# Optimization experiments

Measured on AMD Instinct MI355X. Metric: run time of the kernel, lower is better.

Reference implementation:

```python
import jax, jax.numpy as jnp
import numpy as np

B, H, W, D, DFF = 32, 40, 40, 128, 2048
S = H * W  # 1600
BN_EPS = 1e-5


def setup_inputs() -> dict:
    key = jax.random.key(0)
    ks = jax.random.split(key, 8)
    se = jax.random.normal(ks[2], (H, W, H, W), dtype=jnp.float32)
    se = se + jnp.transpose(se, (2, 3, 0, 1))  # symmetric init as in torch code
    wscale = 0.02
    return {
        "tgt": jax.random.normal(ks[0], (B, H, W, D), dtype=jnp.float32),
        "memory": jax.random.normal(ks[1], (B, H, W, D), dtype=jnp.float32),
        "score_embed": se,
        "w1": jax.random.normal(ks[3], (D, D), dtype=jnp.float32) * wscale,
        "b1": jnp.zeros((D,), jnp.float32),
        "g1": jnp.ones((2 * S,), jnp.float32),
        "be1": jnp.zeros((2 * S,), jnp.float32),
        "w2": jax.random.normal(ks[4], (DFF, 2 * S), dtype=jnp.float32) * wscale,
        "b2": jnp.zeros((DFF,), jnp.float32),
        "g2": jnp.ones((DFF,), jnp.float32),
        "be2": jnp.zeros((DFF,), jnp.float32),
        "w3": jax.random.normal(ks[5], (1, DFF), dtype=jnp.float32) * wscale,
        "b3": jnp.zeros((1,), jnp.float32),
        "g3": jnp.ones((1,), jnp.float32),
        "be3": jnp.zeros((1,), jnp.float32),
    }


def _bn_eval(x, gamma, beta):
    # BatchNorm eval mode with running_mean=0, running_var=1 (as initialized)
    return x * (gamma / jnp.sqrt(1.0 + BN_EPS)) + beta


def _l2norm(x):
    # F.normalize(p=2, dim=-1) with eps=1e-12
    return x / jnp.maximum(jnp.linalg.norm(x, axis=-1, keepdims=True), 1e-12)


def reference(tgt, memory, score_embed, w1, b1, g1, be1, w2, b2, g2, be2, w3, b3, g3, be3):
    b, h, w, d = tgt.shape
    s = h * w
    q = _l2norm(tgt.reshape(b, s, d) @ w1.T + b1)   # [B,S,D]
    k = _l2norm(memory.reshape(b, s, d) @ w1.T + b1)
    gate = jax.nn.sigmoid(score_embed.reshape(s, s))  # [S,S]
    attn = jnp.einsum("bsd,btd->bst", q, k) * gate    # [B,S,S]
    m1 = attn.max(axis=1)  # max over dim 1 -> [B,S]
    m2 = attn.max(axis=2)  # max over dim 2 -> [B,S]
    x = jnp.concatenate([m1, m2], axis=1)  # [B,2S]
    x = _bn_eval(x, g1, be1)
    x = x @ w2.T + b2        # [B,DFF]
    x = jax.nn.relu(_bn_eval(x, g2, be2))
    x = x @ w3.T + b3        # [B,1]
    x = _bn_eval(x, g3, be3)
    return x.squeeze(-1)     # [B]
```

## Files before the change

kernel.cpp:

```cpp
#include <hip/hip_runtime.h>
#include <hip/hip_bf16.h>

#define BB 32
#define SS 1600
#define DD 128
#define DFFN 2048
#define S2N 3200
#define RS 136

typedef __attribute__((ext_vector_type(8))) short short8;
typedef __attribute__((ext_vector_type(4))) float floatx4;
typedef unsigned int u32;
typedef unsigned short u16;

__device__ __forceinline__ u16 f2b(float x) {
  __hip_bfloat16 h = __float2bfloat16(x);
  return __builtin_bit_cast(u16, h);
}
__device__ __forceinline__ float b2f(u16 h) { return __uint_as_float(((u32)h) << 16); }
__device__ __forceinline__ float sigm(float x) { return 1.f / (1.f + __expf(-x)); }
__device__ __forceinline__ short8 pack8(float4 a, float4 b) {
  short8 r;
  r[0] = (short)f2b(a.x); r[1] = (short)f2b(a.y); r[2] = (short)f2b(a.z); r[3] = (short)f2b(a.w);
  r[4] = (short)f2b(b.x); r[5] = (short)f2b(b.y); r[6] = (short)f2b(b.z); r[7] = (short)f2b(b.w);
  return r;
}

__global__ __launch_bounds__(256) void k_prep(const float* __restrict__ tgt,
                                              const float* __restrict__ memin,
                                              const float* __restrict__ w1,
                                              const float* __restrict__ b1,
                                              const float* __restrict__ se,
                                              u16* __restrict__ qb, u16* __restrict__ kb,
                                              u16* __restrict__ gT2) {
  __shared__ u16 sA[128 * RS];
  __shared__ float sq[128];
  int tid = threadIdx.x;
  int lane = tid & 63, wv = tid >> 6;
  int wr = wv >> 1, wc = wv & 1;
  int l15 = lane & 15, lg = lane >> 4;

  if (blockIdx.x >= 800) {
    int bid = blockIdx.x - 800;
    int r2 = bid >> 2, mi = bid & 3;
    int sy = r2 / 13, tx = r2 - sy * 13;
    int s0 = min(sy * 128, SS - 128);
    int t0 = min(tx * 128, SS - 128);
    int srow = s0 + wr * 64 + mi * 16 + lg * 4;
    u16* tb = gT2 + (size_t)r2 * 16384 + wv * 4096 + mi * 4 * 256 + lane * 4;
    for (int ni = 0; ni < 4; ++ni) {
      int tcol = t0 + wc * 64 + ni * 16 + l15;
      const float* sp = se + (size_t)srow * SS + tcol;
      ushort4 o;
      o.x = f2b(sigm(sp[0]));
      o.y = f2b(sigm(sp[SS]));
      o.z = f2b(sigm(sp[2 * SS]));
      o.w = f2b(sigm(sp[3 * SS]));
      *(ushort4*)(tb + ni * 256) = o;
    }
    return;
  }

  long row0 = (long)blockIdx.x * 128;
  const float* src;
  u16* dst;
  if (row0 < (long)BB * SS) { src = tgt + row0 * DD; dst = qb + row0 * DD; }
  else { src = memin + (row0 - (long)BB * SS) * DD; dst = kb + (row0 - (long)BB * SS) * DD; }

  for (int p = 0; p < 16; ++p) {
    int r = p * 8 + (tid >> 5);
    int c4 = (tid & 31) * 4;
    float4 v = *(const float4*)(src + r * DD + c4);
    u32 p0 = (u32)f2b(v.x) | ((u32)f2b(v.y) << 16);
    u32 p1 = (u32)f2b(v.z) | ((u32)f2b(v.w) << 16);
    *(u32*)&sA[r * RS + c4] = p0;
    *(u32*)&sA[r * RS + c4 + 2] = p1;
  }
  if (tid < 128) sq[tid] = 0.f;
  __syncthreads();

  floatx4 acc[4][4];
  for (int mi = 0; mi < 4; ++mi)
    for (int ni = 0; ni < 4; ++ni) acc[mi][ni] = (floatx4){0.f, 0.f, 0.f, 0.f};

  for (int kc = 0; kc < 4; ++kc) {
    int k0 = kc * 32 + lg * 8;
    short8 af[4], bfr[4];
    for (int mi = 0; mi < 4; ++mi) af[mi] = *(const short8*)&sA[(wr * 64 + mi * 16 + l15) * RS + k0];
    for (int ni = 0; ni < 4; ++ni) {
      const float* wp = w1 + (size_t)(wc * 64 + ni * 16 + l15) * DD + k0;
      bfr[ni] = pack8(*(const float4*)wp, *(const float4*)(wp + 4));
    }
    for (int mi = 0; mi < 4; ++mi)
      for (int ni = 0; ni < 4; ++ni)
        acc[mi][ni] = __builtin_amdgcn_mfma_f32_16x16x32_bf16(af[mi], bfr[ni], acc[mi][ni], 0, 0, 0);
  }

  float bvals[4];
  for (int ni = 0; ni < 4; ++ni) bvals[ni] = b1[wc * 64 + ni * 16 + l15];
  for (int mi = 0; mi < 4; ++mi)
    for (int r = 0; r < 4; ++r) {
      float s = 0.f;
      for (int ni = 0; ni < 4; ++ni) {
        float v = acc[mi][ni][r] + bvals[ni];
        acc[mi][ni][r] = v;
        s += v * v;
      }
      s += __shfl_xor(s, 1); s += __shfl_xor(s, 2);
      s += __shfl_xor(s, 4); s += __shfl_xor(s, 8);
      if (l15 == 0) atomicAdd(&sq[wr * 64 + mi * 16 + lg * 4 + r], s);
    }
  __syncthreads();

  for (int mi = 0; mi < 4; ++mi)
    for (int r = 0; r < 4; ++r) {
      int row = wr * 64 + mi * 16 + lg * 4 + r;
      float scale = 1.f / fmaxf(sqrtf(sq[row]), 1e-12f);
      for (int ni = 0; ni < 4; ++ni)
        sA[row * RS + wc * 64 + ni * 16 + l15] = f2b(acc[mi][ni][r] * scale);
    }
  __syncthreads();
  for (int p = 0; p < 16; ++p) {
    int r = p * 8 + (tid >> 5);
    int c4 = (tid & 31) * 4;
    uint2 val = *(const uint2*)&sA[r * RS + c4];
    *(uint2*)(dst + r * DD + c4) = val;
  }
}

__global__ __launch_bounds__(256, 4) void k_attn(const u16* __restrict__ qb,
                                                 const u16* __restrict__ kb,
                                                 const u16* __restrict__ gT2,
                                                 float* __restrict__ p1,
                                                 float* __restrict__ p2) {
  __shared__ u16 sK[128 * RS];
  __shared__ float scmax[2][128];
  __shared__ float srmax[2][128];
  int tid = threadIdx.x;
  int n = blockIdx.x;
  int m = n >> 3;
  int r2 = m >> 2;
  int b = (n & 7) * 4 + (m & 3);
  int sy = r2 / 13, tx = r2 - sy * 13;
  int s0 = min(sy * 128, SS - 128);
  int t0 = min(tx * 128, SS - 128);
  int lane = tid & 63, wv = tid >> 6;
  int wr = wv >> 1, wc = wv & 1;
  int l15 = lane & 15, lg = lane >> 4;
  const size_t base = (size_t)b * SS * DD;
  const u16* qp = qb + base + (size_t)(s0 + wr * 64 + l15) * DD + lg * 8;

  {
    int rr0 = tid >> 4;
    int c8 = (tid & 15) * 8;
    const u16* kp = kb + base + (size_t)(t0 + rr0) * DD + c8;
    u16* sp = &sK[rr0 * RS + c8];
    for (int p = 0; p < 8; ++p)
      *(uint4*)(sp + p * 16 * RS) = *(const uint4*)(kp + (size_t)p * 16 * DD);
  }
  short8 qsA[4], qsB[4];
  for (int mi = 0; mi < 4; ++mi) qsA[mi] = *(const short8*)(qp + mi * 16 * DD);
  __syncthreads();

  floatx4 acc[4][4];
  for (int mi = 0; mi < 4; ++mi)
    for (int ni = 0; ni < 4; ++ni) acc[mi][ni] = (floatx4){0.f, 0.f, 0.f, 0.f};

#define QKSTEP(KC, CUR, NXT, PRE)                                                     \
  {                                                                                   \
    if (PRE)                                                                          \
      for (int mi = 0; mi < 4; ++mi)                                                  \
        NXT[mi] = *(const short8*)(qp + mi * 16 * DD + ((KC) + 1) * 32);              \
    int k0 = (KC)*32 + lg * 8;                                                        \
    short8 bfr[4];                                                                    \
    for (int ni = 0; ni < 4; ++ni)                                                    \
      bfr[ni] = *(const short8*)&sK[(wc * 64 + ni * 16 + l15) * RS + k0];             \
    for (int mi = 0; mi < 4; ++mi)                                                    \
      for (int ni = 0; ni < 4; ++ni)                                                  \
        acc[mi][ni] = __builtin_amdgcn_mfma_f32_16x16x32_bf16(CUR[mi], bfr[ni],       \
                                                              acc[mi][ni], 0, 0, 0);  \
  }
  QKSTEP(0, qsA, qsB, 1)
  QKSTEP(1, qsB, qsA, 1)
  QKSTEP(2, qsA, qsB, 1)
  QKSTEP(3, qsB, qsA, 0)
#undef QKSTEP

  ushort4 gv[4][4];
  {
    const u16* gbase = gT2 + (size_t)r2 * 16384 + wv * 4096 + lane * 4;
    for (int mi = 0; mi < 4; ++mi)
      for (int ni = 0; ni < 4; ++ni)
        gv[mi][ni] = *(const ushort4*)(gbase + (mi * 4 + ni) * 256);
  }

  float rmax[4][4];
  for (int mi = 0; mi < 4; ++mi)
    for (int r = 0; r < 4; ++r) rmax[mi][r] = -1e30f;
  float cmax[4];
  for (int ni = 0; ni < 4; ++ni) cmax[ni] = -1e30f;

  for (int mi = 0; mi < 4; ++mi)
    for (int ni = 0; ni < 4; ++ni) {
      ushort4 ge = gv[mi][ni];
      float v0 = acc[mi][ni][0] * b2f(ge.x);
      float v1 = acc[mi][ni][1] * b2f(ge.y);
      float v2 = acc[mi][ni][2] * b2f(ge.z);
      float v3 = acc[mi][ni][3] * b2f(ge.w);
      rmax[mi][0] = fmaxf(rmax[mi][0], v0);
      rmax[mi][1] = fmaxf(rmax[mi][1], v1);
      rmax[mi][2] = fmaxf(rmax[mi][2], v2);
      rmax[mi][3] = fmaxf(rmax[mi][3], v3);
      cmax[ni] = fmaxf(cmax[ni], fmaxf(fmaxf(v0, v1), fmaxf(v2, v3)));
    }

  for (int ni = 0; ni < 4; ++ni) {
    cmax[ni] = fmaxf(cmax[ni], __shfl_xor(cmax[ni], 16));
    cmax[ni] = fmaxf(cmax[ni], __shfl_xor(cmax[ni], 32));
  }
  if (lane < 16)
    for (int ni = 0; ni < 4; ++ni) scmax[wr][wc * 64 + ni * 16 + lane] = cmax[ni];

  for (int mi = 0; mi < 4; ++mi)
    for (int r = 0; r < 4; ++r) {
      float v = rmax[mi][r];
      v = fmaxf(v, __shfl_xor(v, 1));
      v = fmaxf(v, __shfl_xor(v, 2));
      v = fmaxf(v, __shfl_xor(v, 4));
      v = fmaxf(v, __shfl_xor(v, 8));
      if (l15 == 0) srmax[wc][wr * 64 + mi * 16 + lg * 4 + r] = v;
    }
  __syncthreads();

  size_t pbase = ((size_t)(b * 13 + sy) * 13 + tx) * 128;
  if (tid < 128) {
    p1[pbase + tid] = fmaxf(scmax[0][tid], scmax[1][tid]);
  } else {
    int i2 = tid - 128;
    p2[pbase + i2] = fmaxf(srmax[0][i2], srmax[1][i2]);
  }
}

__global__ __launch_bounds__(256) void k_reduce(const float* __restrict__ p1,
                                                const float* __restrict__ p2,
                                                const float* __restrict__ g1,
                                                const float* __restrict__ be1,
                                                float* __restrict__ xb) {
  int i = blockIdx.x * 256 + threadIdx.x;
  if (i >= BB * S2N) return;
  int bb = i / S2N, c = i - bb * S2N;
  float v = -1e30f;
  if (c < SS) {
    int t = c;
    int txc = min(t >> 7, 12);
    int col = t - ((txc == 12) ? (SS - 128) : txc * 128);
    const float* pp = p1 + ((size_t)(bb * 13) * 13 + txc) * 128 + col;
    for (int sy = 0; sy < 13; ++sy) v = fmaxf(v, pp[(size_t)sy * 13 * 128]);
  } else {
    int s = c - SS;
    int syc = min(s >> 7, 12);
    int col = s - ((syc == 12) ? (SS - 128) : syc * 128);
    const float* pp = p2 + ((size_t)(bb * 13 + syc) * 13) * 128 + col;
    for (int tx = 0; tx < 13; ++tx) v = fmaxf(v, pp[(size_t)tx * 128]);
  }
  float bnc = rsqrtf(1.f + 1e-5f);
  xb[i] = v * (g1[c] * bnc) + be1[c];
}

__global__ __launch_bounds__(256) void k_gemm2(const float* __restrict__ xb,
                                               const float* __restrict__ w2,
                                               float* __restrict__ hacc) {
  int tid = threadIdx.x;
  int lane = tid & 63, wv = tid >> 6;
  int f0 = blockIdx.x * 32 + wv * 8;
  int cs = blockIdx.y;
  int cr0 = cs * 400;
  int c_sub = lane & 15, bq = lane >> 4;
  float acc[8][8];
  for (int a = 0; a < 8; ++a)
    for (int c = 0; c < 8; ++c) acc[a][c] = 0.f;
  const float4 z4 = {0.f, 0.f, 0.f, 0.f};
  for (int it = 0; it < 7; ++it) {
    int coff = it * 64 + c_sub * 4;
    bool ok = coff < 400;
    int c = cr0 + coff;
    float4 w4[8], x4[8];
    for (int jf = 0; jf < 8; ++jf)
      w4[jf] = ok ? *(const float4*)(w2 + (size_t)(f0 + jf) * S2N + c) : z4;
    for (int j = 0; j < 8; ++j)
      x4[j] = ok ? *(const float4*)(xb + (size_t)(bq * 8 + j) * S2N + c) : z4;
    for (int jf = 0; jf < 8; ++jf)
      for (int j = 0; j < 8; ++j) {
        float a = acc[jf][j];
        a = fmaf(w4[jf].x, x4[j].x, a);
        a = fmaf(w4[jf].y, x4[j].y, a);
        a = fmaf(w4[jf].z, x4[j].z, a);
        a = fmaf(w4[jf].w, x4[j].w, a);
        acc[jf][j] = a;
      }
  }
  for (int jf = 0; jf < 8; ++jf)
    for (int j = 0; j < 8; ++j) {
      float v = acc[jf][j];
      v += __shfl_xor(v, 1); v += __shfl_xor(v, 2);
      v += __shfl_xor(v, 4); v += __shfl_xor(v, 8);
      acc[jf][j] = v;
    }
  if ((lane & 15) == 0) {
    for (int jf = 0; jf < 8; ++jf)
      for (int j = 0; j < 8; ++j) {
        int b = bq * 8 + j;
        hacc[((size_t)cs * BB + b) * DFFN + f0 + jf] = acc[jf][j];
      }
  }
}

__global__ __launch_bounds__(256) void k_final(const float* __restrict__ hacc,
                                               const float* __restrict__ b2,
                                               const float* __restrict__ g2,
                                               const float* __restrict__ be2,
                                               const float* __restrict__ w3,
                                               const float* __restrict__ b3,
                                               const float* __restrict__ g3,
                                               const float* __restrict__ be3,
                                               float* __restrict__ out) {
  __shared__ float wsum[4];
  int b = blockIdx.x;
  int tid = threadIdx.x;
  float bnc = rsqrtf(1.f + 1e-5f);
  float part = 0.f;
  for (int f = tid; f < DFFN; f += 256) {
    float s = b2[f];
    for (int cs = 0; cs < 8; ++cs) s += hacc[((size_t)cs * BB + b) * DFFN + f];
    s = s * (g2[f] * bnc) + be2[f];
    s = fmaxf(s, 0.f);
    part += s * w3[f];
  }
  for (int m = 1; m < 64; m <<= 1) part += __shfl_xor(part, m);
  if ((tid & 63) == 0) wsum[tid >> 6] = part;
  __syncthreads();
  if (tid == 0) {
    float tot = wsum[0] + wsum[1] + wsum[2] + wsum[3] + b3[0];
    out[b] = tot * (g3[0] * bnc) + be3[0];
  }
}

extern "C" void kernel_launch(void* const* d_in, const int* in_sizes, int n_in,
                              void* d_out, int out_size, void* d_ws, size_t ws_size,
                              hipStream_t stream) {
  const float* tgt = (const float*)d_in[0];
  const float* memin = (const float*)d_in[1];
  const float* se = (const float*)d_in[2];
  const float* w1 = (const float*)d_in[3];
  const float* b1 = (const float*)d_in[4];
  const float* g1 = (const float*)d_in[5];
  const float* be1 = (const float*)d_in[6];
  const float* w2 = (const float*)d_in[7];
  const float* b2 = (const float*)d_in[8];
  const float* g2 = (const float*)d_in[9];
  const float* be2 = (const float*)d_in[10];
  const float* w3 = (const float*)d_in[11];
  const float* b3 = (const float*)d_in[12];
  const float* g3 = (const float*)d_in[13];
  const float* be3 = (const float*)d_in[14];
  float* out = (float*)d_out;

  char* ws = (char*)d_ws;
  const size_t OFF_GT = 0;
  const size_t OFF_QB = 5537792;
  const size_t OFF_KB = OFF_QB + 13107200;
  const size_t OFF_P1 = OFF_KB + 13107200;
  const size_t OFF_P2 = OFF_P1 + 2768896;
  const size_t NEEDED = OFF_P2 + 2768896;
  const size_t OFF_XB = 0;
  const size_t OFF_HA = 409600;
  if (ws_size < NEEDED) return;

  u16* gT2 = (u16*)(ws + OFF_GT);
  u16* qb = (u16*)(ws + OFF_QB);
  u16* kb = (u16*)(ws + OFF_KB);
  float* p1 = (float*)(ws + OFF_P1);
  float* p2 = (float*)(ws + OFF_P2);
  float* xb = (float*)(ws + OFF_XB);
  float* hacc = (float*)(ws + OFF_HA);

  k_prep<<<1476, 256, 0, stream>>>(tgt, memin, w1, b1, se, qb, kb, gT2);
  k_attn<<<5408, 256, 0, stream>>>(qb, kb, gT2, p1, p2);
  k_reduce<<<400, 256, 0, stream>>>(p1, p2, g1, be1, xb);
  k_gemm2<<<dim3(64, 8), 256, 0, stream>>>(xb, w2, hacc);
  k_final<<<32, 256, 0, stream>>>(hacc, b2, g2, be2, w3, b3, g3, be3, out);
}
```

Measured before the change: 148.6 us.

## Replace partial-max buffers and reduce kernel with atomicMax, fuse BN1 into gemm2

The attention kernel now merges its per-tile row and column maxima straight into per-batch arrays with atomicMax. Floats are encoded as order-preserving unsigned ints, and the arrays are zeroed inside the prep kernel. This removes the partial-max buffers and the separate k_reduce launch. The first batch-norm is applied inside gemm2 while it decodes the maxima. The gate tile layout is also repacked so each lane loads it with eight 16-byte loads instead of sixteen 8-byte loads. The cost is atomic contention on each output element, about 13 updates per element, plus decode arithmetic in gemm2.

```diff
diff --git a/kernel.cpp b/kernel.cpp
--- a/kernel.cpp
+++ b/kernel.cpp
@@ -13,11 +13,18 @@
 typedef unsigned int u32;
 typedef unsigned short u16;
 
+__device__ __forceinline__ u32 encf(float f) {
+  u32 u = __float_as_uint(f);
+  return (u & 0x80000000u) ? ~u : (u | 0x80000000u);
+}
+__device__ __forceinline__ float decf(u32 e) {
+  u32 u = (e & 0x80000000u) ? (e & 0x7fffffffu) : ~e;
+  return __uint_as_float(u);
+}
 __device__ __forceinline__ u16 f2b(float x) {
   __hip_bfloat16 h = __float2bfloat16(x);
   return __builtin_bit_cast(u16, h);
 }
-__device__ __forceinline__ float b2f(u16 h) { return __uint_as_float(((u32)h) << 16); }
 __device__ __forceinline__ float sigm(float x) { return 1.f / (1.f + __expf(-x)); }
 __device__ __forceinline__ short8 pack8(float4 a, float4 b) {
   short8 r;
@@ -32,7 +39,8 @@
                                               const float* __restrict__ b1,
                                               const float* __restrict__ se,
                                               u16* __restrict__ qb, u16* __restrict__ kb,
-                                              u16* __restrict__ gT2) {
+                                              u16* __restrict__ gT2,
+                                              u32* __restrict__ m1u, u32* __restrict__ m2u) {
   __shared__ u16 sA[128 * RS];
   __shared__ float sq[128];
   int tid = threadIdx.x;
@@ -42,12 +50,17 @@
 
   if (blockIdx.x >= 800) {
     int bid = blockIdx.x - 800;
+    int ii = bid * 256 + tid;
+    if (ii < BB * SS) {
+      m1u[ii] = 0u;
+      m2u[ii] = 0u;
+    }
     int r2 = bid >> 2, mi = bid & 3;
     int sy = r2 / 13, tx = r2 - sy * 13;
     int s0 = min(sy * 128, SS - 128);
     int t0 = min(tx * 128, SS - 128);
     int srow = s0 + wr * 64 + mi * 16 + lg * 4;
-    u16* tb = gT2 + (size_t)r2 * 16384 + wv * 4096 + mi * 4 * 256 + lane * 4;
+    u16* tb = gT2 + (size_t)r2 * 16384 + wv * 4096 + lane * 8;
     for (int ni = 0; ni < 4; ++ni) {
       int tcol = t0 + wc * 64 + ni * 16 + l15;
       const float* sp = se + (size_t)srow * SS + tcol;
@@ -56,7 +69,7 @@
       o.y = f2b(sigm(sp[SS]));
       o.z = f2b(sigm(sp[2 * SS]));
       o.w = f2b(sigm(sp[3 * SS]));
-      *(ushort4*)(tb + ni * 256) = o;
+      *(ushort4*)(tb + (mi * 2 + (ni >> 1)) * 512 + (ni & 1) * 4) = o;
     }
     return;
   }
@@ -131,8 +144,7 @@
 __global__ __launch_bounds__(256, 4) void k_attn(const u16* __restrict__ qb,
                                                  const u16* __restrict__ kb,
                                                  const u16* __restrict__ gT2,
-                                                 float* __restrict__ p1,
-                                                 float* __restrict__ p2) {
+                                                 u32* __restrict__ m1u, u32* __restrict__ m2u) {
   __shared__ u16 sK[128 * RS];
   __shared__ float scmax[2][128];
   __shared__ float srmax[2][128];
@@ -186,12 +198,10 @@
   QKSTEP(3, qsB, qsA, 0)
 #undef QKSTEP
 
-  ushort4 gv[4][4];
+  uint4 g4[8];
   {
-    const u16* gbase = gT2 + (size_t)r2 * 16384 + wv * 4096 + lane * 4;
-    for (int mi = 0; mi < 4; ++mi)
-      for (int ni = 0; ni < 4; ++ni)
-        gv[mi][ni] = *(const ushort4*)(gbase + (mi * 4 + ni) * 256);
+    const u16* gbase = gT2 + (size_t)r2 * 16384 + wv * 4096 + lane * 8;
+    for (int p = 0; p < 8; ++p) g4[p] = *(const uint4*)(gbase + p * 512);
   }
 
   float rmax[4][4];
@@ -202,11 +212,13 @@
 
   for (int mi = 0; mi < 4; ++mi)
     for (int ni = 0; ni < 4; ++ni) {
-      ushort4 ge = gv[mi][ni];
-      float v0 = acc[mi][ni][0] * b2f(ge.x);
-      float v1 = acc[mi][ni][1] * b2f(ge.y);
-      float v2 = acc[mi][ni][2] * b2f(ge.z);
-      float v3 = acc[mi][ni][3] * b2f(ge.w);
+      uint4 pg = g4[mi * 2 + (ni >> 1)];
+      u32 lo = (ni & 1) ? pg.z : pg.x;
+      u32 hi = (ni & 1) ? pg.w : pg.y;
+      float v0 = acc[mi][ni][0] * __uint_as_float(lo << 16);
+      float v1 = acc[mi][ni][1] * __uint_as_float(lo & 0xffff0000u);
+      float v2 = acc[mi][ni][2] * __uint_as_float(hi << 16);
+      float v3 = acc[mi][ni][3] * __uint_as_float(hi & 0xffff0000u);
       rmax[mi][0] = fmaxf(rmax[mi][0], v0);
       rmax[mi][1] = fmaxf(rmax[mi][1], v1);
       rmax[mi][2] = fmaxf(rmax[mi][2], v2);
@@ -232,42 +244,20 @@
     }
   __syncthreads();
 
-  size_t pbase = ((size_t)(b * 13 + sy) * 13 + tx) * 128;
   if (tid < 128) {
-    p1[pbase + tid] = fmaxf(scmax[0][tid], scmax[1][tid]);
+    float v = fmaxf(scmax[0][tid], scmax[1][tid]);
+    atomicMax(&m1u[b * SS + t0 + tid], encf(v));
   } else {
     int i2 = tid - 128;
-    p2[pbase + i2] = fmaxf(srmax[0][i2], srmax[1][i2]);
-  }
-}
-
-__global__ __launch_bounds__(256) void k_reduce(const float* __restrict__ p1,
-                                                const float* __restrict__ p2,
-                                                const float* __restrict__ g1,
-                                                const float* __restrict__ be1,
-                                                float* __restrict__ xb) {
-  int i = blockIdx.x * 256 + threadIdx.x;
-  if (i >= BB * S2N) return;
-  int bb = i / S2N, c = i - bb * S2N;
-  float v = -1e30f;
-  if (c < SS) {
-    int t = c;
-    int txc = min(t >> 7, 12);
-    int col = t - ((txc == 12) ? (SS - 128) : txc * 128);
-    const float* pp = p1 + ((size_t)(bb * 13) * 13 + txc) * 128 + col;
-    for (int sy = 0; sy < 13; ++sy) v = fmaxf(v, pp[(size_t)sy * 13 * 128]);
-  } else {
-    int s = c - SS;
-    int syc = min(s >> 7, 12);
-    int col = s - ((syc == 12) ? (SS - 128) : syc * 128);
-    const float* pp = p2 + ((size_t)(bb * 13 + syc) * 13) * 128 + col;
-    for (int tx = 0; tx < 13; ++tx) v = fmaxf(v, pp[(size_t)tx * 128]);
-  }
-  float bnc = rsqrtf(1.f + 1e-5f);
-  xb[i] = v * (g1[c] * bnc) + be1[c];
-}
-
-__global__ __launch_bounds__(256) void k_gemm2(const float* __restrict__ xb,
+    float v = fmaxf(srmax[0][i2], srmax[1][i2]);
+    atomicMax(&m2u[b * SS + s0 + i2], encf(v));
+  }
+}
+
+__global__ __launch_bounds__(256) void k_gemm2(const u32* __restrict__ m1u,
+                                               const u32* __restrict__ m2u,
+                                               const float* __restrict__ g1,
+                                               const float* __restrict__ be1,
                                                const float* __restrict__ w2,
                                                float* __restrict__ hacc) {
   int tid = threadIdx.x;
@@ -275,7 +265,10 @@
   int f0 = blockIdx.x * 32 + wv * 8;
   int cs = blockIdx.y;
   int cr0 = cs * 400;
+  const u32* msrc = (cs < 4) ? m1u : m2u;
+  int mcol0 = cr0 - ((cs < 4) ? 0 : SS);
   int c_sub = lane & 15, bq = lane >> 4;
+  const float bnc = rsqrtf(1.f + 1e-5f);
   float acc[8][8];
   for (int a = 0; a < 8; ++a)
     for (int c = 0; c < 8; ++c) acc[a][c] = 0.f;
@@ -283,12 +276,24 @@
   for (int it = 0; it < 7; ++it) {
     int coff = it * 64 + c_sub * 4;
     bool ok = coff < 400;
-    int c = cr0 + coff;
+    int cg = cr0 + coff;
     float4 w4[8], x4[8];
+    float4 gv = ok ? *(const float4*)(g1 + cg) : z4;
+    float4 bv = ok ? *(const float4*)(be1 + cg) : z4;
+    gv.x *= bnc; gv.y *= bnc; gv.z *= bnc; gv.w *= bnc;
     for (int jf = 0; jf < 8; ++jf)
-      w4[jf] = ok ? *(const float4*)(w2 + (size_t)(f0 + jf) * S2N + c) : z4;
-    for (int j = 0; j < 8; ++j)
-      x4[j] = ok ? *(const float4*)(xb + (size_t)(bq * 8 + j) * S2N + c) : z4;
+      w4[jf] = ok ? *(const float4*)(w2 + (size_t)(f0 + jf) * S2N + cg) : z4;
+    for (int j = 0; j < 8; ++j) {
+      if (ok) {
+        uint4 e = *(const uint4*)(msrc + (size_t)(bq * 8 + j) * SS + mcol0 + coff);
+        x4[j].x = decf(e.x) * gv.x + bv.x;
+        x4[j].y = decf(e.y) * gv.y + bv.y;
+        x4[j].z = decf(e.z) * gv.z + bv.z;
+        x4[j].w = decf(e.w) * gv.w + bv.w;
+      } else {
+        x4[j] = z4;
+      }
+    }
     for (int jf = 0; jf < 8; ++jf)
       for (int j = 0; j < 8; ++j) {
         float a = acc[jf][j];
@@ -369,24 +374,21 @@
   const size_t OFF_GT = 0;
   const size_t OFF_QB = 5537792;
   const size_t OFF_KB = OFF_QB + 13107200;
-  const size_t OFF_P1 = OFF_KB + 13107200;
-  const size_t OFF_P2 = OFF_P1 + 2768896;
-  const size_t NEEDED = OFF_P2 + 2768896;
-  const size_t OFF_XB = 0;
-  const size_t OFF_HA = 409600;
+  const size_t OFF_M1 = OFF_KB + 13107200;
+  const size_t OFF_M2 = OFF_M1 + 204800;
+  const size_t OFF_HA = OFF_M2 + 204800;
+  const size_t NEEDED = OFF_HA + 2097152;
   if (ws_size < NEEDED) return;
 
   u16* gT2 = (u16*)(ws + OFF_GT);
   u16* qb = (u16*)(ws + OFF_QB);
   u16* kb = (u16*)(ws + OFF_KB);
-  float* p1 = (float*)(ws + OFF_P1);
-  float* p2 = (float*)(ws + OFF_P2);
-  float* xb = (float*)(ws + OFF_XB);
+  u32* m1u = (u32*)(ws + OFF_M1);
+  u32* m2u = (u32*)(ws + OFF_M2);
   float* hacc = (float*)(ws + OFF_HA);
 
-  k_prep<<<1476, 256, 0, stream>>>(tgt, memin, w1, b1, se, qb, kb, gT2);
-  k_attn<<<5408, 256, 0, stream>>>(qb, kb, gT2, p1, p2);
-  k_reduce<<<400, 256, 0, stream>>>(p1, p2, g1, be1, xb);
-  k_gemm2<<<dim3(64, 8), 256, 0, stream>>>(xb, w2, hacc);
+  k_prep<<<1476, 256, 0, stream>>>(tgt, memin, w1, b1, se, qb, kb, gT2, m1u, m2u);
+  k_attn<<<5408, 256, 0, stream>>>(qb, kb, gT2, m1u, m2u);
+  k_gemm2<<<dim3(64, 8), 256, 0, stream>>>(m1u, m2u, g1, be1, w2, hacc);
   k_final<<<32, 256, 0, stream>>>(hacc, b2, g2, be2, w3, b3, g3, be3, out);
 }
```

Result: faster. 144.1 us (-3.0%).
